# Optimization experiments

Measured on AMD Instinct MI355X. Metric: run time of the kernel, lower is better.

The kernel has to match this reference:

```python
import jax, jax.numpy as jnp
import numpy as np

MARGIN = 0.3
N_CLASSES = 1024
N_SAMPLES = 32
D = 512


def setup_inputs() -> dict:
    key = jax.random.key(0)
    k1, k2 = jax.random.split(key)
    embeddings = jax.random.normal(k1, (2 * N_CLASSES * N_SAMPLES, D), dtype=jnp.float32)
    target = jax.random.randint(k2, (2 * N_CLASSES * N_SAMPLES,), 0, N_CLASSES, dtype=jnp.int64)
    return {"embeddings": embeddings, "target": target}


def reference(embeddings, target):
    # [C, 2, S, D]: per class, block 0 = positives, block 1 = negatives
    e = embeddings.reshape(N_CLASSES, 2, N_SAMPLES, D)
    pos = e[:, 0]  # [C, S, D]
    neg = e[:, 1]  # [C, S, D]
    anchor = pos.mean(axis=1, keepdims=True)  # [C, 1, D]
    ap = jnp.sum((anchor - pos) ** 2, axis=-1)  # [C, S]
    neg_d = jnp.sum((neg - anchor) ** 2, axis=-1)  # [C, S]
    # an_distances = dist(anchor, nearest negative) == min over negatives
    an = jnp.min(neg_d, axis=1, keepdims=True)  # [C, 1]
    losses = jnp.sum(jax.nn.relu(ap - an + MARGIN), axis=1)  # [C]
    return losses.mean()
```

## Files before the change

kernel.cpp:

```cpp
#include <hip/hip_runtime.h>

#define NC 1024
#define NS 32
#define DD 512
#define MARGIN 0.3f

__global__ __launch_bounds__(512) void ccl_per_class(const float* __restrict__ emb,
                                                     float* __restrict__ cls) {
    const int c = blockIdx.x;
    const int t = threadIdx.x;
    const int lane = t & 63;
    const int wv = t >> 6;
    const float* pos = emb + (size_t)c * (2 * NS * DD);
    const float* neg = pos + NS * DD;

    __shared__ float s_wap[8][32];
    __shared__ float s_wnd[8][32];

    float p[32], n[32];
#pragma unroll
    for (int s = 0; s < 32; ++s) p[s] = pos[s * DD + t];
#pragma unroll
    for (int s = 0; s < 32; ++s) n[s] = neg[s * DD + t];

    float a = 0.f;
#pragma unroll
    for (int s = 0; s < 32; ++s) a += p[s];
    a *= (1.f / NS);

#pragma unroll
    for (int s = 0; s < 32; ++s) { float d = p[s] - a; p[s] = d * d; }
#pragma unroll
    for (int s = 0; s < 32; ++s) { float d = n[s] - a; n[s] = d * d; }

#define BSTEP(arr, m, half)                                        \
    {                                                              \
        _Pragma("unroll")                                          \
        for (int i = 0; i < (half); ++i) {                         \
            float lo = arr[i], hi = arr[i + (half)];               \
            float send = (lane & (m)) ? lo : hi;                   \
            float recv = __shfl_xor(send, (m));                    \
            arr[i] = (lane & (m)) ? (hi + recv) : (lo + recv);     \
        }                                                          \
    }
    BSTEP(p, 1, 16) BSTEP(p, 2, 8) BSTEP(p, 4, 4) BSTEP(p, 8, 2) BSTEP(p, 16, 1)
    BSTEP(n, 1, 16) BSTEP(n, 2, 8) BSTEP(n, 4, 4) BSTEP(n, 8, 2) BSTEP(n, 16, 1)
#undef BSTEP
    float rap = p[0] + __shfl_xor(p[0], 32);
    float rnd = n[0] + __shfl_xor(n[0], 32);
    if (lane < 32) {
        const int jm = ((lane & 1) << 4) | ((lane & 2) << 2) | (lane & 4) |
                       ((lane & 8) >> 2) | ((lane & 16) >> 4);
        s_wap[wv][jm] = rap;
        s_wnd[wv][jm] = rnd;
    }
    __syncthreads();

    if (t < NS) {
        float ap = 0.f, nd = 0.f;
#pragma unroll
        for (int w = 0; w < 8; ++w) { ap += s_wap[w][t]; nd += s_wnd[w][t]; }
        float an = nd;
#pragma unroll
        for (int m = 1; m < 32; m <<= 1) an = fminf(an, __shfl_xor(an, m));
        float l = fmaxf(ap - an + MARGIN, 0.f);
#pragma unroll
        for (int m = 1; m < 32; m <<= 1) l += __shfl_xor(l, m);
        if (t == 0) cls[c] = l;
    }
}

__global__ __launch_bounds__(256) void ccl_reduce(const float* __restrict__ class_loss,
                                                  float* __restrict__ out) {
    const int t = threadIdx.x;
    float v = class_loss[t] + class_loss[t + 256] + class_loss[t + 512] + class_loss[t + 768];
#pragma unroll
    for (int m = 32; m >= 1; m >>= 1) v += __shfl_down(v, m);
    __shared__ float s_partial[4];
    if ((t & 63) == 0) s_partial[t >> 6] = v;
    __syncthreads();
    if (t == 0)
        out[0] = (s_partial[0] + s_partial[1] + s_partial[2] + s_partial[3]) * (1.f / NC);
}

extern "C" void kernel_launch(void* const* d_in, const int* in_sizes, int n_in,
                              void* d_out, int out_size, void* d_ws, size_t ws_size,
                              hipStream_t stream) {
    const float* emb = (const float*)d_in[0];
    float* cls = (float*)d_ws;
    float* out = (float*)d_out;
    ccl_per_class<<<NC, 512, 0, stream>>>(emb, cls);
    ccl_reduce<<<1, 256, 0, stream>>>(cls, out);
}
```

Measured before the change: 29.42 us.

## Split samples across two thread groups with 1024-thread blocks

After: 31.99 us. +8.7%, slower.

```diff
diff --git a/kernel.cpp b/kernel.cpp
--- a/kernel.cpp
+++ b/kernel.cpp
@@ -5,33 +5,38 @@
 #define DD 512
 #define MARGIN 0.3f
 
-__global__ __launch_bounds__(512) void ccl_per_class(const float* __restrict__ emb,
-                                                     float* __restrict__ cls) {
+__global__ __launch_bounds__(1024) void ccl_per_class(const float* __restrict__ emb,
+                                                      float* __restrict__ cls) {
     const int c = blockIdx.x;
     const int t = threadIdx.x;
+    const int g = t >> 9;
+    const int col = t & 511;
     const int lane = t & 63;
     const int wv = t >> 6;
     const float* pos = emb + (size_t)c * (2 * NS * DD);
     const float* neg = pos + NS * DD;
 
-    __shared__ float s_wap[8][32];
-    __shared__ float s_wnd[8][32];
+    __shared__ float s_part[2][DD];
+    __shared__ float s_wap[16][16];
+    __shared__ float s_wnd[16][16];
 
-    float p[32], n[32];
+    float p[16], n[16];
 #pragma unroll
-    for (int s = 0; s < 32; ++s) p[s] = pos[s * DD + t];
+    for (int j = 0; j < 16; ++j) p[j] = pos[(2 * j + g) * DD + col];
 #pragma unroll
-    for (int s = 0; s < 32; ++s) n[s] = neg[s * DD + t];
+    for (int j = 0; j < 16; ++j) n[j] = neg[(2 * j + g) * DD + col];
 
-    float a = 0.f;
+    float a = p[0];
 #pragma unroll
-    for (int s = 0; s < 32; ++s) a += p[s];
-    a *= (1.f / NS);
+    for (int j = 1; j < 16; ++j) a += p[j];
+    s_part[g][col] = a;
+    __syncthreads();
+    a = (s_part[0][col] + s_part[1][col]) * (1.f / NS);
 
 #pragma unroll
-    for (int s = 0; s < 32; ++s) { float d = p[s] - a; p[s] = d * d; }
+    for (int j = 0; j < 16; ++j) { float d = p[j] - a; p[j] = d * d; }
 #pragma unroll
-    for (int s = 0; s < 32; ++s) { float d = n[s] - a; n[s] = d * d; }
+    for (int j = 0; j < 16; ++j) { float d = n[j] - a; n[j] = d * d; }
 
 #define BSTEP(arr, m, half)                                        \
     {                                                              \
@@ -43,23 +48,30 @@
             arr[i] = (lane & (m)) ? (hi + recv) : (lo + recv);     \
         }                                                          \
     }
-    BSTEP(p, 1, 16) BSTEP(p, 2, 8) BSTEP(p, 4, 4) BSTEP(p, 8, 2) BSTEP(p, 16, 1)
-    BSTEP(n, 1, 16) BSTEP(n, 2, 8) BSTEP(n, 4, 4) BSTEP(n, 8, 2) BSTEP(n, 16, 1)
+    BSTEP(p, 1, 8) BSTEP(p, 2, 4) BSTEP(p, 4, 2) BSTEP(p, 8, 1)
+    BSTEP(n, 1, 8) BSTEP(n, 2, 4) BSTEP(n, 4, 2) BSTEP(n, 8, 1)
 #undef BSTEP
-    float rap = p[0] + __shfl_xor(p[0], 32);
-    float rnd = n[0] + __shfl_xor(n[0], 32);
-    if (lane < 32) {
-        const int jm = ((lane & 1) << 4) | ((lane & 2) << 2) | (lane & 4) |
-                       ((lane & 8) >> 2) | ((lane & 16) >> 4);
+    float rap = p[0];
+    rap += __shfl_xor(rap, 16);
+    rap += __shfl_xor(rap, 32);
+    float rnd = n[0];
+    rnd += __shfl_xor(rnd, 16);
+    rnd += __shfl_xor(rnd, 32);
+    if (lane < 16) {
+        const int jm = ((lane & 1) << 3) | ((lane & 2) << 1) | ((lane & 4) >> 1) | ((lane & 8) >> 3);
         s_wap[wv][jm] = rap;
         s_wnd[wv][jm] = rnd;
     }
     __syncthreads();
 
     if (t < NS) {
+        const int sg = t & 1, sj = t >> 1;
         float ap = 0.f, nd = 0.f;
 #pragma unroll
-        for (int w = 0; w < 8; ++w) { ap += s_wap[w][t]; nd += s_wnd[w][t]; }
+        for (int k = 0; k < 8; ++k) {
+            ap += s_wap[sg * 8 + k][sj];
+            nd += s_wnd[sg * 8 + k][sj];
+        }
         float an = nd;
 #pragma unroll
         for (int m = 1; m < 32; m <<= 1) an = fminf(an, __shfl_xor(an, m));
@@ -89,6 +101,6 @@
     const float* emb = (const float*)d_in[0];
     float* cls = (float*)d_ws;
     float* out = (float*)d_out;
-    ccl_per_class<<<NC, 512, 0, stream>>>(emb, cls);
+    ccl_per_class<<<NC, 1024, 0, stream>>>(emb, cls);
     ccl_reduce<<<1, 256, 0, stream>>>(cls, out);
 }
```

## Vectorize per-class loads as float4 and split samples across thread groups

Applied to the files above, without the earlier changes.

After: 27.15 us. 1.08x faster.

```diff
diff --git a/kernel.cpp b/kernel.cpp
--- a/kernel.cpp
+++ b/kernel.cpp
@@ -9,29 +9,48 @@
                                                      float* __restrict__ cls) {
     const int c = blockIdx.x;
     const int t = threadIdx.x;
+    const int g = t >> 7;
+    const int col4 = t & 127;
     const int lane = t & 63;
     const int wv = t >> 6;
-    const float* pos = emb + (size_t)c * (2 * NS * DD);
-    const float* neg = pos + NS * DD;
+    const float4* posv = (const float4*)(emb + (size_t)c * (2 * NS * DD));
+    const float4* negv = posv + NS * DD / 4;
 
-    __shared__ float s_wap[8][32];
-    __shared__ float s_wnd[8][32];
+    __shared__ float4 s_part[4][128];
+    __shared__ float s_wap[8][8];
+    __shared__ float s_wnd[8][8];
 
-    float p[32], n[32];
+    float4 p[8], n[8];
 #pragma unroll
-    for (int s = 0; s < 32; ++s) p[s] = pos[s * DD + t];
+    for (int j = 0; j < 8; ++j) p[j] = posv[(4 * j + g) * (DD / 4) + col4];
 #pragma unroll
-    for (int s = 0; s < 32; ++s) n[s] = neg[s * DD + t];
+    for (int j = 0; j < 8; ++j) n[j] = negv[(4 * j + g) * (DD / 4) + col4];
 
-    float a = 0.f;
+    float4 acc = p[0];
 #pragma unroll
-    for (int s = 0; s < 32; ++s) a += p[s];
-    a *= (1.f / NS);
+    for (int j = 1; j < 8; ++j) {
+        acc.x += p[j].x; acc.y += p[j].y; acc.z += p[j].z; acc.w += p[j].w;
+    }
+    s_part[g][col4] = acc;
+    __syncthreads();
+    float4 a;
+    {
+        float4 x0 = s_part[0][col4], x1 = s_part[1][col4];
+        float4 x2 = s_part[2][col4], x3 = s_part[3][col4];
+        a.x = (x0.x + x1.x + x2.x + x3.x) * (1.f / NS);
+        a.y = (x0.y + x1.y + x2.y + x3.y) * (1.f / NS);
+        a.z = (x0.z + x1.z + x2.z + x3.z) * (1.f / NS);
+        a.w = (x0.w + x1.w + x2.w + x3.w) * (1.f / NS);
+    }
 
+    float apc[8], ndc[8];
 #pragma unroll
-    for (int s = 0; s < 32; ++s) { float d = p[s] - a; p[s] = d * d; }
-#pragma unroll
-    for (int s = 0; s < 32; ++s) { float d = n[s] - a; n[s] = d * d; }
+    for (int j = 0; j < 8; ++j) {
+        float dx = p[j].x - a.x, dy = p[j].y - a.y, dz = p[j].z - a.z, dw = p[j].w - a.w;
+        apc[j] = dx * dx + dy * dy + dz * dz + dw * dw;
+        dx = n[j].x - a.x; dy = n[j].y - a.y; dz = n[j].z - a.z; dw = n[j].w - a.w;
+        ndc[j] = dx * dx + dy * dy + dz * dz + dw * dw;
+    }
 
 #define BSTEP(arr, m, half)                                        \
     {                                                              \
@@ -43,23 +62,28 @@
             arr[i] = (lane & (m)) ? (hi + recv) : (lo + recv);     \
         }                                                          \
     }
-    BSTEP(p, 1, 16) BSTEP(p, 2, 8) BSTEP(p, 4, 4) BSTEP(p, 8, 2) BSTEP(p, 16, 1)
-    BSTEP(n, 1, 16) BSTEP(n, 2, 8) BSTEP(n, 4, 4) BSTEP(n, 8, 2) BSTEP(n, 16, 1)
+    BSTEP(apc, 1, 4) BSTEP(apc, 2, 2) BSTEP(apc, 4, 1)
+    BSTEP(ndc, 1, 4) BSTEP(ndc, 2, 2) BSTEP(ndc, 4, 1)
 #undef BSTEP
-    float rap = p[0] + __shfl_xor(p[0], 32);
-    float rnd = n[0] + __shfl_xor(n[0], 32);
-    if (lane < 32) {
-        const int jm = ((lane & 1) << 4) | ((lane & 2) << 2) | (lane & 4) |
-                       ((lane & 8) >> 2) | ((lane & 16) >> 4);
+    float rap = apc[0];
+    rap += __shfl_xor(rap, 8);
+    rap += __shfl_xor(rap, 16);
+    rap += __shfl_xor(rap, 32);
+    float rnd = ndc[0];
+    rnd += __shfl_xor(rnd, 8);
+    rnd += __shfl_xor(rnd, 16);
+    rnd += __shfl_xor(rnd, 32);
+    if (lane < 8) {
+        const int jm = ((lane & 1) << 2) | (lane & 2) | ((lane & 4) >> 2);
         s_wap[wv][jm] = rap;
         s_wnd[wv][jm] = rnd;
     }
     __syncthreads();
 
     if (t < NS) {
-        float ap = 0.f, nd = 0.f;
-#pragma unroll
-        for (int w = 0; w < 8; ++w) { ap += s_wap[w][t]; nd += s_wnd[w][t]; }
+        const int sg = t & 3, sj = t >> 2;
+        float ap = s_wap[sg * 2][sj] + s_wap[sg * 2 + 1][sj];
+        float nd = s_wnd[sg * 2][sj] + s_wnd[sg * 2 + 1][sj];
         float an = nd;
 #pragma unroll
         for (int m = 1; m < 32; m <<= 1) an = fminf(an, __shfl_xor(an, m));
```
